# Kernel optimization log

Measured on AMD Instinct MI355X. Metric: run time of the kernel, lower is better.

Reference implementation:

```python
import jax, jax.numpy as jnp
import numpy as np

N, E = 20000, 4096
IN_DIM, DET_DIM, HID, OUT = 512, 256, 256, 2
HALF = HID // 2
EPS = 1e-6


def setup_inputs() -> dict:
    key = jax.random.key(0)
    ks = jax.random.split(key, 20)
    g = lambda k, shape, fan_in: jax.random.normal(k, shape, jnp.float32) / np.sqrt(fan_in)
    return {
        "x": jax.random.normal(ks[0], (N, IN_DIM), jnp.float32),
        "z": jax.random.normal(ks[1], (N, DET_DIM), jnp.float32),
        "incidence": jax.random.uniform(ks[2], (N, E), jnp.float32),
        "edge_weights": jax.random.uniform(ks[3], (E,), jnp.float32),
        "psi_w": g(ks[4], (IN_DIM, HALF), IN_DIM), "psi_b": jnp.zeros((HALF,), jnp.float32),
        "phi_w": g(ks[5], (DET_DIM, HALF), DET_DIM), "phi_b": jnp.zeros((HALF,), jnp.float32),
        "g1_w": g(ks[6], (2 * HALF, HID), 2 * HALF), "g1_b": jnp.zeros((HID,), jnp.float32),
        "g2_w": g(ks[7], (HID, HALF), HID), "g2_b": jnp.zeros((HALF,), jnp.float32),
        "th1": g(ks[8], (HALF, HID), HALF), "b1": jnp.zeros((HID,), jnp.float32),
        "th2": g(ks[9], (HID, HID), HID), "b2": jnp.zeros((HID,), jnp.float32),
        "out_w": g(ks[10], (HID, OUT), HID), "out_b": jnp.zeros((OUT,), jnp.float32),
    }


def hconv(X, H, w, theta, bias):
    # HGNN-style message passing: Dv^{-1/2} H W De^{-1} H^T Dv^{-1/2} (X theta) + b
    Xt = X @ theta                              # [N,F]
    De = H.sum(axis=0)                          # [E] edge degree
    Dv = H @ w                                  # [N] weighted node degree
    inv_sqrt_dv = jax.lax.rsqrt(jnp.maximum(Dv, EPS))[:, None]
    He = H.T @ (Xt * inv_sqrt_dv)               # [E,F] gather to hyperedges
    He = He * (w / jnp.maximum(De, EPS))[:, None]
    return (H @ He) * inv_sqrt_dv + bias        # scatter back to nodes


def reference(x, z, incidence, edge_weights,
              psi_w, psi_b, phi_w, phi_b,
              g1_w, g1_b, g2_w, g2_b,
              th1, b1, th2, b2, out_w, out_b):
    proj_x = x @ psi_w + psi_b                  # [N,HALF]
    proj_z = z @ phi_w + phi_b                  # [N,HALF]
    cat = jnp.concatenate([proj_x, proj_z], axis=1)
    gate = jax.nn.sigmoid(jax.nn.relu(cat @ g1_w + g1_b) @ g2_w + g2_b)
    fused = gate * proj_z + (1.0 - gate) * proj_x
    h = jax.nn.relu(hconv(fused, incidence, edge_weights, th1, b1))
    h = jax.nn.relu(hconv(h, incidence, edge_weights, th2, b2))
    logits = h @ out_w + out_b                  # [N,OUT]
    return logits, gate
```

## Files before the change

### kernel.cpp

```cpp
#include <hip/hip_runtime.h>
#include <hip/hip_bf16.h>


typedef __bf16 bf16_t;
typedef __attribute__((ext_vector_type(8))) __bf16 bf16x8;
typedef __attribute__((ext_vector_type(4))) __bf16 bf16x4;
typedef __attribute__((ext_vector_type(4))) float f32x4;

#define NN 20000
#define NE 4096
#define NNP 20480
#define AT_S 16
#define NEB 8
#define NNB 160

__device__ __forceinline__ f32x4 mfma16(bf16x8 a, bf16x8 b, f32x4 c) {
  return __builtin_amdgcn_mfma_f32_16x16x32_bf16(a, b, c, 0, 0, 0);
}

__global__ __launch_bounds__(256) void stats_cvt_kern(const float* __restrict__ H,
                                                      const float* __restrict__ w,
                                                      float* __restrict__ Dvp,
                                                      float* __restrict__ Dep,
                                                      bf16_t* __restrict__ Hbp) {
  __shared__ float dvl[128][17];
  __shared__ float deP[4][512];
  int t = threadIdx.x, l = t & 63, wv = t >> 6;
  long e0 = (long)blockIdx.x * 512;
  long n0 = (long)blockIdx.y * 128;
  long pA = ((e0 >> 6) + (l >> 4)) * (long)NNP;
  long pB = pA + 4 * (long)NNP;
  int inner = (l & 15) * 4;
  f32x4 wa = *(const f32x4*)(w + e0 + l * 4);
  f32x4 wb = *(const f32x4*)(w + e0 + 256 + l * 4);
  f32x4 dea; dea[0] = dea[1] = dea[2] = dea[3] = 0.f;
  f32x4 deb; deb[0] = deb[1] = deb[2] = deb[3] = 0.f;
  #pragma unroll 4
  for (int i = 0; i < 32; ++i) {
    long row = n0 + wv * 32 + i;
    float s;
    if (row < NN) {
      f32x4 ua = *(const f32x4*)(H + row * NE + e0 + l * 4);
      f32x4 ub = *(const f32x4*)(H + row * NE + e0 + 256 + l * 4);
      bf16x4 pa, pb;
      #pragma unroll
      for (int j = 0; j < 4; ++j) { pa[j] = (__bf16)ua[j]; pb[j] = (__bf16)ub[j]; }
      *(bf16x4*)(Hbp + (pA + row) * 64 + inner) = pa;
      *(bf16x4*)(Hbp + (pB + row) * 64 + inner) = pb;
      dea += ua; deb += ub;
      s = ua[0]*wa[0] + ua[1]*wa[1] + ua[2]*wa[2] + ua[3]*wa[3]
        + ub[0]*wb[0] + ub[1]*wb[1] + ub[2]*wb[2] + ub[3]*wb[3];
    } else {
      bf16x4 z;
      #pragma unroll
      for (int j = 0; j < 4; ++j) z[j] = (__bf16)0.f;
      *(bf16x4*)(Hbp + (pA + row) * 64 + inner) = z;
      *(bf16x4*)(Hbp + (pB + row) * 64 + inner) = z;
      s = 0.f;
    }
    s += __shfl_xor(s, 1);
    s += __shfl_xor(s, 2);
    if ((l & 3) == 0) dvl[wv * 32 + i][l >> 2] = s;
  }
  *(f32x4*)(&deP[wv][l * 4]) = dea;
  *(f32x4*)(&deP[wv][256 + l * 4]) = deb;
  __syncthreads();
  if (t < 128) {
    float s = 0.f;
    #pragma unroll
    for (int j = 0; j < 16; ++j) s += dvl[t][j];
    Dvp[(long)blockIdx.x * NNP + n0 + t] = s;
  }
  {
    float s0 = deP[0][t] + deP[1][t] + deP[2][t] + deP[3][t];
    float s1 = deP[0][256 + t] + deP[1][256 + t] + deP[2][256 + t] + deP[3][256 + t];
    Dep[(long)blockIdx.y * NE + e0 + t] = s0;
    Dep[(long)blockIdx.y * NE + e0 + 256 + t] = s1;
  }
}

__global__ __launch_bounds__(256) void finalize_kern(const float* __restrict__ Dvp,
                                                     const float* __restrict__ Dep,
                                                     const float* __restrict__ w,
                                                     float* __restrict__ isd,
                                                     float* __restrict__ es) {
  int t = blockIdx.x * 256 + threadIdx.x;
  if (t < NN) {
    float s = 0.f;
    #pragma unroll
    for (int b = 0; b < NEB; ++b) s += Dvp[(long)b * NNP + t];
    isd[t] = rsqrtf(fmaxf(s, 1e-6f));
  }
  if (t < NE) {
    float s = 0.f;
    #pragma unroll 8
    for (int b = 0; b < NNB; ++b) s += Dep[(long)b * NE + t];
    es[t] = w[t] / fmaxf(s, 1e-6f);
  }
}

__global__ void cvtw_kern(const float* __restrict__ psi, const float* __restrict__ phi,
                          const float* __restrict__ g1,  const float* __restrict__ g2,
                          const float* __restrict__ th1, const float* __restrict__ th2,
                          bf16_t* dpsi, bf16_t* dphi, bf16_t* dg1, bf16_t* dg2,
                          bf16_t* dth1, bf16_t* dth2) {
  int t = blockIdx.x * 256 + threadIdx.x;
  if (t < 65536) {
    int nc = t >> 9, k = t & 511; dpsi[t] = (__bf16)psi[k * 128 + nc];
  } else if (t < 98304) {
    int i = t - 65536; int nc = i >> 8, k = i & 255; dphi[i] = (__bf16)phi[k * 128 + nc];
  } else if (t < 163840) {
    int i = t - 98304; int nc = i >> 8, k = i & 255; dg1[i] = (__bf16)g1[k * 256 + nc];
  } else if (t < 196608) {
    int i = t - 163840; int nc = i >> 8, k = i & 255; dg2[i] = (__bf16)g2[k * 128 + nc];
  } else if (t < 229376) {
    int i = t - 196608; int nc = i >> 7, k = i & 127; dth1[i] = (__bf16)th1[k * 256 + nc];
  } else if (t < 294912) {
    int i = t - 229376; int nc = i >> 8, k = i & 255; dth2[i] = (__bf16)th2[k * 256 + nc];
  }
}

enum { EPI_CAT = 0, EPI_RELU = 1 };

template<bool AF32, int EPI>
__global__ __launch_bounds__(256) void gemm_node_kern(
    const void* __restrict__ Av, int lda, const bf16_t* __restrict__ Bt, int K,
    const float* __restrict__ bias, bf16_t* __restrict__ dst, int ldc) {
  int tid = threadIdx.x, l = tid & 63, wv = tid >> 6;
  int lr = l & 15, lq = l >> 4;
  int hm = wv >> 1;
  int mo = blockIdx.x * 32 + hm * 16;
  int no = blockIdx.y * 128 + (wv & 1) * 64;
  f32x4 acc[4] = {};
  for (int k0 = 0; k0 < K; k0 += 32) {
    int row = mo + lr;
    bf16x8 a;
    if (row < NN) {
      if constexpr (AF32) {
        const float* ap = (const float*)Av + (long)row * lda + k0 + lq * 8;
        f32x4 u0 = *(const f32x4*)ap, u1 = *(const f32x4*)(ap + 4);
        #pragma unroll
        for (int j = 0; j < 4; ++j) { a[j] = (__bf16)u0[j]; a[j + 4] = (__bf16)u1[j]; }
      } else {
        a = *(const bf16x8*)((const bf16_t*)Av + (long)row * lda + k0 + lq * 8);
      }
    } else {
      #pragma unroll
      for (int j = 0; j < 8; ++j) a[j] = (__bf16)0.f;
    }
    #pragma unroll
    for (int ni = 0; ni < 4; ++ni) {
      bf16x8 b = *(const bf16x8*)(Bt + (long)(no + ni * 16 + lr) * K + k0 + lq * 8);
      acc[ni] = mfma16(a, b, acc[ni]);
    }
  }
  #pragma unroll
  for (int ni = 0; ni < 4; ++ni) {
    int colf = no + ni * 16 + lr;
    int rb = mo + lq * 4;
    f32x4 v = acc[ni];
    float bs = bias[colf];
    for (int r = 0; r < 4; ++r) {
      int n = rb + r;
      if (n < NN) {
        float xx = v[r] + bs;
        if constexpr (EPI == EPI_RELU) xx = xx > 0.f ? xx : 0.f;
        dst[(long)n * ldc + colf] = (__bf16)xx;
      }
    }
  }
}

__global__ __launch_bounds__(256) void gate_y_kern(
    const bf16_t* __restrict__ hid1, const bf16_t* __restrict__ g2w,
    const float* __restrict__ g2b, const bf16_t* __restrict__ cat,
    const bf16_t* __restrict__ th1w, const float* __restrict__ isd,
    float* __restrict__ gate_out, bf16_t* __restrict__ Yf) {
  __shared__ bf16_t fl[32 * 132];
  int t = threadIdx.x, l = t & 63, wv = t >> 6;
  int lr = l & 15, lq = l >> 4;
  if (blockIdx.x >= 625) {
    bf16x8 z;
    #pragma unroll
    for (int j = 0; j < 8; ++j) z[j] = (__bf16)0.f;
    #pragma unroll
    for (int i = 0; i < 4; ++i)
      *(bf16x8*)(Yf + (((long)(wv + i * 4) * 640 + blockIdx.x) * 64 + l) * 8) = z;
    return;
  }
  long n0 = (long)blockIdx.x * 32;
  int hm = wv >> 1, nq = wv & 1;
  int mo = hm * 16, no = nq * 64;
  f32x4 acc[4] = {};
  for (int k0 = 0; k0 < 256; k0 += 32) {
    bf16x8 a = *(const bf16x8*)(hid1 + (n0 + mo + lr) * 256 + k0 + lq * 8);
    #pragma unroll
    for (int ni = 0; ni < 4; ++ni) {
      bf16x8 b = *(const bf16x8*)(g2w + (long)(no + ni * 16 + lr) * 256 + k0 + lq * 8);
      acc[ni] = mfma16(a, b, acc[ni]);
    }
  }
  #pragma unroll
  for (int ni = 0; ni < 4; ++ni) {
    int colf = no + ni * 16 + lr;
    float bs = g2b[colf];
    #pragma unroll
    for (int r = 0; r < 4; ++r) {
      long n = n0 + mo + lq * 4 + r;
      float g = 1.f / (1.f + __expf(-(acc[ni][r] + bs)));
      gate_out[n * 128 + colf] = g;
      float px = (float)cat[n * 256 + colf];
      float pz = (float)cat[n * 256 + 128 + colf];
      fl[(mo + lq * 4 + r) * 132 + colf] = (__bf16)(g * pz + (1.f - g) * px);
    }
  }
  __syncthreads();
  int hm2 = wv >> 1, f128 = (wv & 1) * 128;
  f32x4 acc2[8] = {};
  for (int k0 = 0; k0 < 128; k0 += 32) {
    bf16x8 a = *(const bf16x8*)(fl + (hm2 * 16 + lr) * 132 + k0 + lq * 8);
    #pragma unroll
    for (int ni = 0; ni < 8; ++ni) {
      bf16x8 b = *(const bf16x8*)(th1w + (long)(f128 + ni * 16 + lr) * 128 + k0 + lq * 8);
      acc2[ni] = mfma16(a, b, acc2[ni]);
    }
  }
  int lanep = (hm2 * 2 + (lq >> 1)) * 16 + lr;
  #pragma unroll
  for (int ni = 0; ni < 8; ++ni) {
    int fblk = (f128 >> 4) + ni;
    bf16x4 pk;
    #pragma unroll
    for (int r = 0; r < 4; ++r) {
      long n = n0 + hm2 * 16 + lq * 4 + r;
      pk[r] = (__bf16)(acc2[ni][r] * isd[n]);
    }
    *(bf16x4*)(Yf + (((long)fblk * 640 + blockIdx.x) * 64 + lanep) * 8 + (lq & 1) * 4) = pk;
  }
}

__global__ __launch_bounds__(512) void at_gemm_kern(const bf16_t* __restrict__ Hbp,
                                                    const bf16_t* __restrict__ Yf,
                                                    bf16_t* __restrict__ part) {
  __shared__ bf16_t T[128 * 72];
  int t = threadIdx.x, l = t & 63, wv = t >> 6;
  int lr = l & 15, lq = l >> 4;
  int eh = wv >> 2, fq = wv & 3;
  int e0 = blockIdx.x * 128;
  int s0 = blockIdx.y * 20, s1 = s0 + 20;
  int rp = t >> 4;
  int ck = t & 15;
  f32x4 acc[4][4] = {};
  const bf16_t* src = Hbp + (((long)(e0 >> 6) + (ck >> 3)) * NNP + (long)s0 * 64 + 2 * rp) * 64
                          + (ck & 7) * 8;
  bf16x8 ra = *(const bf16x8*)src;
  bf16x8 rb = *(const bf16x8*)(src + 64);
  for (int s = s0; s < s1; ++s) {
    __syncthreads();
    #pragma unroll
    for (int j = 0; j < 8; ++j) {
      int jj = (j + ck) & 7;
      int el = ck * 8 + jj;
      unsigned lo = (unsigned)__builtin_bit_cast(unsigned short, (__bf16)ra[jj]);
      unsigned hi = (unsigned)__builtin_bit_cast(unsigned short, (__bf16)rb[jj]);
      *(unsigned*)(T + el * 72 + rp * 2) = lo | (hi << 16);
    }
    __syncthreads();
    if (s + 1 < s1) {
      src += 64 * 64;
      ra = *(const bf16x8*)src;
      rb = *(const bf16x8*)(src + 64);
    }
    #pragma unroll
    for (int k32 = 0; k32 < 2; ++k32) {
      bf16x8 a[4], b[4];
      #pragma unroll
      for (int ni = 0; ni < 4; ++ni)
        a[ni] = *(const bf16x8*)(T + (eh * 64 + ni * 16 + lr) * 72 + k32 * 32 + lq * 8);
      const bf16_t* bp = Yf + ((long)(s * 2 + k32) * 64 + l) * 8;
      #pragma unroll
      for (int ni = 0; ni < 4; ++ni)
        b[ni] = *(const bf16x8*)(bp + (long)(fq * 4 + ni) * 640 * 512);
      #pragma unroll
      for (int ae = 0; ae < 4; ++ae)
        #pragma unroll
        for (int bf = 0; bf < 4; ++bf)
          acc[ae][bf] = mfma16(a[ae], b[bf], acc[ae][bf]);
    }
  }
  bf16_t* pp = part + (long)blockIdx.y * (256 * 4096);
  #pragma unroll
  for (int ae = 0; ae < 4; ++ae) {
    int eblk16 = (e0 >> 4) + eh * 4 + ae;
    #pragma unroll
    for (int bf = 0; bf < 4; ++bf) {
      int fblk = fq * 4 + bf;
      f32x4 v = acc[ae][bf];
      bf16x4 pk;
      for (int r = 0; r < 4; ++r) pk[r] = (__bf16)v[r];
      *(bf16x4*)(pp + (((long)eblk16 * 16 + fblk) * 64 + l) * 4) = pk;
    }
  }
}

__global__ __launch_bounds__(256) void reduce_he(const bf16_t* __restrict__ part,
                                                 const float* __restrict__ es,
                                                 bf16_t* __restrict__ Hef) {
  int u = blockIdx.x * 256 + threadIdx.x;
  int lane = u & 63, tile = u >> 6;
  int fblk = tile & 15, eblk16 = tile >> 4;
  int lr = lane & 15, lq = lane >> 4;
  int e_base = eblk16 * 16 + lq * 4;
  float a0 = 0.f, a1 = 0.f, a2 = 0.f, a3 = 0.f;
  #pragma unroll
  for (int s = 0; s < AT_S; ++s) {
    bf16x4 v = *(const bf16x4*)(part + (long)s * (256 * 4096) + (long)u * 4);
    a0 += (float)v[0]; a1 += (float)v[1]; a2 += (float)v[2]; a3 += (float)v[3];
  }
  f32x4 e4 = *(const f32x4*)(es + e_base);
  bf16x4 pk;
  pk[0] = (__bf16)(a0 * e4[0]); pk[1] = (__bf16)(a1 * e4[1]);
  pk[2] = (__bf16)(a2 * e4[2]); pk[3] = (__bf16)(a3 * e4[3]);
  int eblk32 = eblk16 >> 1;
  int lanep = ((eblk16 & 1) * 2 + (lq >> 1)) * 16 + lr;
  long slot = (((long)fblk * 128 + eblk32) * 64 + lanep) * 8 + (lq & 1) * 4;
  *(bf16x4*)(Hef + slot) = pk;
}

template<int CONV>
__global__ __launch_bounds__(512) void out_gemm_kern(const bf16_t* __restrict__ Hef,
                                                     const bf16_t* __restrict__ Hbp,
                                                     const float* __restrict__ isd,
                                                     const float* __restrict__ bias,
                                                     const bf16_t* __restrict__ th2w,
                                                     bf16_t* __restrict__ Yf,
                                                     const float* __restrict__ ow,
                                                     const float* __restrict__ ob,
                                                     float* __restrict__ out) {
  __shared__ bf16_t lbuf[2][5120];
  __shared__ float lgp[8][80][2];
  __shared__ bf16_t hl[80 * 260];
  int t = threadIdx.x, l = t & 63, wv = t >> 6;
  int lr = l & 15, lq = l >> 4;
  long r0 = (long)blockIdx.x * 80;
  f32x4 acc[5][2] = {};
  int f1 = wv, f2 = 8 + wv;
  bool has2 = wv < 2;
  const bf16_t* asrc1 = Hbp + (r0 + (f1 >> 1) * 16 + lr) * 64 + (f1 & 1) * 32 + lq * 8;
  const bf16_t* asrc2 = Hbp + (r0 + (f2 >> 1) * 16 + lr) * 64 + (f2 & 1) * 32 + lq * 8;
  const bf16_t* bbase = Hef + (long)l * 8;
  bf16x8 rg1 = *(const bf16x8*)asrc1;
  bf16x8 rg2;
  if (has2) rg2 = *(const bf16x8*)asrc2;
  int c = 0;
  for (int s = 0; s < 64; ++s) {
    *(bf16x8*)(&lbuf[c][f1 * 512 + l * 8]) = rg1;
    if (has2) *(bf16x8*)(&lbuf[c][f2 * 512 + l * 8]) = rg2;
    __syncthreads();
    if (s + 1 < 64) {
      rg1 = *(const bf16x8*)(asrc1 + (long)(s + 1) * NNP * 64);
      if (has2) rg2 = *(const bf16x8*)(asrc2 + (long)(s + 1) * NNP * 64);
    }
    #pragma unroll
    for (int k32 = 0; k32 < 2; ++k32) {
      bf16x8 a[5], b[2];
      #pragma unroll
      for (int mi = 0; mi < 5; ++mi)
        a[mi] = *(const bf16x8*)(&lbuf[c][(mi * 2 + k32) * 512 + l * 8]);
      int eblk = s * 2 + k32;
      #pragma unroll
      for (int ni = 0; ni < 2; ++ni)
        b[ni] = *(const bf16x8*)(bbase + ((long)(wv * 2 + ni) * 128 + eblk) * 512);
      #pragma unroll
      for (int mi = 0; mi < 5; ++mi) {
        acc[mi][0] = mfma16(a[mi], b[0], acc[mi][0]);
        acc[mi][1] = mfma16(a[mi], b[1], acc[mi][1]);
      }
    }
    c ^= 1;
  }
  #pragma unroll
  for (int mi = 0; mi < 5; ++mi) {
    long nb = r0 + mi * 16 + lq * 4;
    #pragma unroll
    for (int r = 0; r < 4; ++r) {
      long n = nb + r;
      float sd = (n < NN) ? isd[n] : 0.f;
      float a0 = 0.f, a1 = 0.f;
      #pragma unroll
      for (int ni = 0; ni < 2; ++ni) {
        int f = wv * 32 + ni * 16 + lr;
        float vv = acc[mi][ni][r] * sd + bias[f];
        vv = vv > 0.f ? vv : 0.f;
        if constexpr (CONV == 1) {
          hl[(mi * 16 + lq * 4 + r) * 260 + f] = (__bf16)vv;
        } else {
          a0 += vv * ow[f * 2];
          a1 += vv * ow[f * 2 + 1];
        }
      }
      if constexpr (CONV == 2) {
        #pragma unroll
        for (int m = 1; m < 16; m <<= 1) { a0 += __shfl_xor(a0, m); a1 += __shfl_xor(a1, m); }
        if (lr == 0) {
          int rowl = mi * 16 + lq * 4 + r;
          lgp[wv][rowl][0] = a0;
          lgp[wv][rowl][1] = a1;
        }
      }
    }
  }
  if constexpr (CONV == 1) {
    __syncthreads();
    f32x4 acc2[5][2] = {};
    for (int k0 = 0; k0 < 256; k0 += 32) {
      bf16x8 a_[5], b2[2];
      #pragma unroll
      for (int mi = 0; mi < 5; ++mi)
        a_[mi] = *(const bf16x8*)(hl + (mi * 16 + lr) * 260 + k0 + lq * 8);
      #pragma unroll
      for (int ni = 0; ni < 2; ++ni)
        b2[ni] = *(const bf16x8*)(th2w + (long)(wv * 32 + ni * 16 + lr) * 256 + k0 + lq * 8);
      #pragma unroll
      for (int mi = 0; mi < 5; ++mi) {
        acc2[mi][0] = mfma16(a_[mi], b2[0], acc2[mi][0]);
        acc2[mi][1] = mfma16(a_[mi], b2[1], acc2[mi][1]);
      }
    }
    #pragma unroll
    for (int mi = 0; mi < 5; ++mi) {
      long nbase = r0 + mi * 16;
      long nblk = nbase >> 5;
      int hm16 = (int)((nbase >> 4) & 1);
      int lanep = (hm16 * 2 + (lq >> 1)) * 16 + lr;
      #pragma unroll
      for (int ni = 0; ni < 2; ++ni) {
        int fblk = wv * 2 + ni;
        bf16x4 pk;
        #pragma unroll
        for (int r = 0; r < 4; ++r) {
          long n = nbase + lq * 4 + r;
          float sc = (n < NN) ? isd[n] : 0.f;
          pk[r] = (__bf16)(acc2[mi][ni][r] * sc);
        }
        *(bf16x4*)(Yf + (((long)fblk * 640 + nblk) * 64 + lanep) * 8 + (lq & 1) * 4) = pk;
      }
    }
  } else {
    __syncthreads();
    if (t < 80) {
      float s0 = 0.f, s1 = 0.f;
      #pragma unroll
      for (int wvi = 0; wvi < 8; ++wvi) { s0 += lgp[wvi][t][0]; s1 += lgp[wvi][t][1]; }
      long n = r0 + t;
      if (n < NN) {
        out[n * 2]     = s0 + ob[0];
        out[n * 2 + 1] = s1 + ob[1];
      }
    }
  }
}

extern "C" void kernel_launch(void* const* d_in, const int* in_sizes, int n_in,
                              void* d_out, int out_size, void* d_ws, size_t ws_size,
                              hipStream_t stream) {
  const float* x    = (const float*)d_in[0];
  const float* z    = (const float*)d_in[1];
  const float* H    = (const float*)d_in[2];
  const float* w    = (const float*)d_in[3];
  const float* psi_w = (const float*)d_in[4];
  const float* psi_b = (const float*)d_in[5];
  const float* phi_w = (const float*)d_in[6];
  const float* phi_b = (const float*)d_in[7];
  const float* g1_w  = (const float*)d_in[8];
  const float* g1_b  = (const float*)d_in[9];
  const float* g2_w  = (const float*)d_in[10];
  const float* g2_b  = (const float*)d_in[11];
  const float* th1   = (const float*)d_in[12];
  const float* b1    = (const float*)d_in[13];
  const float* th2   = (const float*)d_in[14];
  const float* b2    = (const float*)d_in[15];
  const float* out_w = (const float*)d_in[16];
  const float* out_b = (const float*)d_in[17];

  float* logits_out = (float*)d_out;
  float* gate_out   = logits_out + (size_t)NN * 2;

  char* p = (char*)d_ws;
  auto alloc = [&](size_t bytes) { char* r = p; p += (bytes + 255) & ~(size_t)255; return r; };
  float* Dvp  = (float*)alloc((size_t)NEB * NNP * 4);
  float* Dep  = (float*)alloc((size_t)NNB * NE * 4);
  float* isd  = (float*)alloc((size_t)NN * 4);
  float* es   = (float*)alloc((size_t)NE * 4);
  bf16_t* cat   = (bf16_t*)alloc((size_t)NN * 256 * 2);
  bf16_t* hid1  = (bf16_t*)alloc((size_t)NN * 256 * 2);
  bf16_t* Yf    = (bf16_t*)alloc((size_t)16 * 640 * 512 * 2);
  bf16_t* Hef   = (bf16_t*)alloc((size_t)16 * 128 * 512 * 2);
  bf16_t* pbuf  = (bf16_t*)alloc((size_t)AT_S * 256 * 4096 * 2);
  bf16_t* Hbp   = (bf16_t*)alloc((size_t)NNP * NE * 2);
  bf16_t* psi_wt = (bf16_t*)alloc(65536 * 2);
  bf16_t* phi_wt = (bf16_t*)alloc(32768 * 2);
  bf16_t* g1_wt  = (bf16_t*)alloc(65536 * 2);
  bf16_t* g2_wt  = (bf16_t*)alloc(32768 * 2);
  bf16_t* th1_wt = (bf16_t*)alloc(32768 * 2);
  bf16_t* th2_wt = (bf16_t*)alloc(65536 * 2);

  cvtw_kern<<<1152, 256, 0, stream>>>(psi_w, phi_w, g1_w, g2_w, th1, th2,
                                      psi_wt, phi_wt, g1_wt, g2_wt, th1_wt, th2_wt);
  stats_cvt_kern<<<dim3(NEB, NNB), 256, 0, stream>>>(H, w, Dvp, Dep, Hbp);
  finalize_kern<<<79, 256, 0, stream>>>(Dvp, Dep, w, isd, es);

  gemm_node_kern<true,  EPI_CAT ><<<dim3(625, 1), 256, 0, stream>>>(x, 512, psi_wt, 512, psi_b, cat,       256);
  gemm_node_kern<true,  EPI_CAT ><<<dim3(625, 1), 256, 0, stream>>>(z, 256, phi_wt, 256, phi_b, cat + 128, 256);
  gemm_node_kern<false, EPI_RELU><<<dim3(625, 2), 256, 0, stream>>>(cat, 256, g1_wt, 256, g1_b, hid1, 256);
  gate_y_kern<<<640, 256, 0, stream>>>(hid1, g2_wt, g2_b, cat, th1_wt, isd, gate_out, Yf);

  at_gemm_kern<<<dim3(32, AT_S), 512, 0, stream>>>(Hbp, Yf, pbuf);
  reduce_he<<<1024, 256, 0, stream>>>(pbuf, es, Hef);
  out_gemm_kern<1><<<256, 512, 0, stream>>>(Hef, Hbp, isd, b1, th2_wt, Yf,
                                            nullptr, nullptr, nullptr);

  at_gemm_kern<<<dim3(32, AT_S), 512, 0, stream>>>(Hbp, Yf, pbuf);
  reduce_he<<<1024, 256, 0, stream>>>(pbuf, es, Hef);
  out_gemm_kern<2><<<256, 512, 0, stream>>>(Hef, Hbp, isd, b2, nullptr, nullptr,
                                            out_w, out_b, logits_out);

  (void)in_sizes; (void)n_in; (void)out_size; (void)ws_size;
}
```

Measured before the change: 537.1 us.

## Merge independent prologue kernels and double-buffer LDS in hyperedge gather GEMM

The incidence-stats/bf16 conversion kernel is merged with the x/z projection GEMMs into one launch. The degree finalize step is merged with the gate hidden GEMM into a second launch, dispatched by block index. This cuts the kernel count and lets the independent work overlap. Separately, the at_gemm kernel now double-buffers its LDS transpose tile, so each step needs one barrier instead of two and the next tile's write overlaps the current MFMAs. The cost is twice the LDS in at_gemm, which could lower occupancy.

```diff
diff --git a/kernel.cpp b/kernel.cpp
--- a/kernel.cpp
+++ b/kernel.cpp
@@ -18,16 +18,13 @@
   return __builtin_amdgcn_mfma_f32_16x16x32_bf16(a, b, c, 0, 0, 0);
 }
 
-__global__ __launch_bounds__(256) void stats_cvt_kern(const float* __restrict__ H,
-                                                      const float* __restrict__ w,
-                                                      float* __restrict__ Dvp,
-                                                      float* __restrict__ Dep,
-                                                      bf16_t* __restrict__ Hbp) {
-  __shared__ float dvl[128][17];
-  __shared__ float deP[4][512];
+__device__ __forceinline__ void stats_body(int vbx, int vby,
+    const float* __restrict__ H, const float* __restrict__ w,
+    float* __restrict__ Dvp, float* __restrict__ Dep, bf16_t* __restrict__ Hbp,
+    float (*dvl)[17], float (*deP)[512]) {
   int t = threadIdx.x, l = t & 63, wv = t >> 6;
-  long e0 = (long)blockIdx.x * 512;
-  long n0 = (long)blockIdx.y * 128;
+  long e0 = (long)vbx * 512;
+  long n0 = (long)vby * 128;
   long pA = ((e0 >> 6) + (l >> 4)) * (long)NNP;
   long pB = pA + 4 * (long)NNP;
   int inner = (l & 15) * 4;
@@ -69,33 +66,131 @@
     float s = 0.f;
     #pragma unroll
     for (int j = 0; j < 16; ++j) s += dvl[t][j];
-    Dvp[(long)blockIdx.x * NNP + n0 + t] = s;
+    Dvp[(long)vbx * NNP + n0 + t] = s;
   }
   {
     float s0 = deP[0][t] + deP[1][t] + deP[2][t] + deP[3][t];
     float s1 = deP[0][256 + t] + deP[1][256 + t] + deP[2][256 + t] + deP[3][256 + t];
-    Dep[(long)blockIdx.y * NE + e0 + t] = s0;
-    Dep[(long)blockIdx.y * NE + e0 + 256 + t] = s1;
-  }
-}
-
-__global__ __launch_bounds__(256) void finalize_kern(const float* __restrict__ Dvp,
-                                                     const float* __restrict__ Dep,
-                                                     const float* __restrict__ w,
-                                                     float* __restrict__ isd,
-                                                     float* __restrict__ es) {
-  int t = blockIdx.x * 256 + threadIdx.x;
-  if (t < NN) {
-    float s = 0.f;
-    #pragma unroll
-    for (int b = 0; b < NEB; ++b) s += Dvp[(long)b * NNP + t];
-    isd[t] = rsqrtf(fmaxf(s, 1e-6f));
-  }
-  if (t < NE) {
-    float s = 0.f;
-    #pragma unroll 8
-    for (int b = 0; b < NNB; ++b) s += Dep[(long)b * NE + t];
-    es[t] = w[t] / fmaxf(s, 1e-6f);
+    Dep[(long)vby * NE + e0 + t] = s0;
+    Dep[(long)vby * NE + e0 + 256 + t] = s1;
+  }
+}
+
+__device__ __forceinline__ void cat_gemm_body(const float* __restrict__ Av, int lda,
+    const bf16_t* __restrict__ Bt, int K, const float* __restrict__ bias,
+    bf16_t* __restrict__ dst, int vbx) {
+  int tid = threadIdx.x, l = tid & 63, wv = tid >> 6;
+  int lr = l & 15, lq = l >> 4;
+  int mo = vbx * 32 + (wv >> 1) * 16;
+  int no = (wv & 1) * 64;
+  f32x4 acc[4] = {};
+  for (int k0 = 0; k0 < K; k0 += 32) {
+    int row = mo + lr;
+    bf16x8 a;
+    if (row < NN) {
+      const float* ap = Av + (long)row * lda + k0 + lq * 8;
+      f32x4 u0 = *(const f32x4*)ap, u1 = *(const f32x4*)(ap + 4);
+      #pragma unroll
+      for (int j = 0; j < 4; ++j) { a[j] = (__bf16)u0[j]; a[j + 4] = (__bf16)u1[j]; }
+    } else {
+      #pragma unroll
+      for (int j = 0; j < 8; ++j) a[j] = (__bf16)0.f;
+    }
+    #pragma unroll
+    for (int ni = 0; ni < 4; ++ni) {
+      bf16x8 b = *(const bf16x8*)(Bt + (long)(no + ni * 16 + lr) * K + k0 + lq * 8);
+      acc[ni] = mfma16(a, b, acc[ni]);
+    }
+  }
+  #pragma unroll
+  for (int ni = 0; ni < 4; ++ni) {
+    int colf = no + ni * 16 + lr;
+    int rb = mo + lq * 4;
+    float bs = bias[colf];
+    #pragma unroll
+    for (int r = 0; r < 4; ++r) {
+      int n = rb + r;
+      if (n < NN) dst[(long)n * 256 + colf] = (__bf16)(acc[ni][r] + bs);
+    }
+  }
+}
+
+__global__ __launch_bounds__(256) void fusedA_kern(const float* __restrict__ H,
+    const float* __restrict__ w, float* __restrict__ Dvp, float* __restrict__ Dep,
+    bf16_t* __restrict__ Hbp,
+    const float* __restrict__ x, const bf16_t* __restrict__ psi_wt,
+    const float* __restrict__ psi_b,
+    const float* __restrict__ z, const bf16_t* __restrict__ phi_wt,
+    const float* __restrict__ phi_b, bf16_t* __restrict__ cat) {
+  __shared__ float dvl[128][17];
+  __shared__ float deP[4][512];
+  int bid = blockIdx.x;
+  if (bid < 1280) {
+    stats_body(bid & 7, bid >> 3, H, w, Dvp, Dep, Hbp, dvl, deP);
+  } else if (bid < 1905) {
+    cat_gemm_body(x, 512, psi_wt, 512, psi_b, cat, bid - 1280);
+  } else {
+    cat_gemm_body(z, 256, phi_wt, 256, phi_b, cat + 128, bid - 1905);
+  }
+}
+
+__global__ __launch_bounds__(256) void fusedB_kern(const float* __restrict__ Dvp,
+    const float* __restrict__ Dep, const float* __restrict__ w,
+    float* __restrict__ isd, float* __restrict__ es,
+    const bf16_t* __restrict__ cat, const bf16_t* __restrict__ g1w,
+    const float* __restrict__ g1b, bf16_t* __restrict__ hid1) {
+  int bid = blockIdx.x;
+  if (bid < 79) {
+    int t = bid * 256 + threadIdx.x;
+    if (t < NN) {
+      float s = 0.f;
+      #pragma unroll
+      for (int b = 0; b < NEB; ++b) s += Dvp[(long)b * NNP + t];
+      isd[t] = rsqrtf(fmaxf(s, 1e-6f));
+    }
+    if (t < NE) {
+      float s = 0.f;
+      #pragma unroll 8
+      for (int b = 0; b < NNB; ++b) s += Dep[(long)b * NE + t];
+      es[t] = w[t] / fmaxf(s, 1e-6f);
+    }
+    return;
+  }
+  int i = bid - 79;
+  int vbx = i % 625, vby = i / 625;
+  int tid = threadIdx.x, l = tid & 63, wv = tid >> 6;
+  int lr = l & 15, lq = l >> 4;
+  int mo = vbx * 32 + (wv >> 1) * 16;
+  int no = vby * 128 + (wv & 1) * 64;
+  f32x4 acc[4] = {};
+  for (int k0 = 0; k0 < 256; k0 += 32) {
+    int row = mo + lr;
+    bf16x8 a;
+    if (row < NN) {
+      a = *(const bf16x8*)(cat + (long)row * 256 + k0 + lq * 8);
+    } else {
+      #pragma unroll
+      for (int j = 0; j < 8; ++j) a[j] = (__bf16)0.f;
+    }
+    #pragma unroll
+    for (int ni = 0; ni < 4; ++ni) {
+      bf16x8 b = *(const bf16x8*)(g1w + (long)(no + ni * 16 + lr) * 256 + k0 + lq * 8);
+      acc[ni] = mfma16(a, b, acc[ni]);
+    }
+  }
+  #pragma unroll
+  for (int ni = 0; ni < 4; ++ni) {
+    int colf = no + ni * 16 + lr;
+    int rb = mo + lq * 4;
+    float bs = g1b[colf];
+    #pragma unroll
+    for (int r = 0; r < 4; ++r) {
+      int n = rb + r;
+      if (n < NN) {
+        float xx = acc[ni][r] + bs;
+        hid1[(long)n * 256 + colf] = (__bf16)(xx > 0.f ? xx : 0.f);
+      }
+    }
   }
 }
 
@@ -120,57 +215,6 @@
   }
 }
 
-enum { EPI_CAT = 0, EPI_RELU = 1 };
-
-template<bool AF32, int EPI>
-__global__ __launch_bounds__(256) void gemm_node_kern(
-    const void* __restrict__ Av, int lda, const bf16_t* __restrict__ Bt, int K,
-    const float* __restrict__ bias, bf16_t* __restrict__ dst, int ldc) {
-  int tid = threadIdx.x, l = tid & 63, wv = tid >> 6;
-  int lr = l & 15, lq = l >> 4;
-  int hm = wv >> 1;
-  int mo = blockIdx.x * 32 + hm * 16;
-  int no = blockIdx.y * 128 + (wv & 1) * 64;
-  f32x4 acc[4] = {};
-  for (int k0 = 0; k0 < K; k0 += 32) {
-    int row = mo + lr;
-    bf16x8 a;
-    if (row < NN) {
-      if constexpr (AF32) {
-        const float* ap = (const float*)Av + (long)row * lda + k0 + lq * 8;
-        f32x4 u0 = *(const f32x4*)ap, u1 = *(const f32x4*)(ap + 4);
-        #pragma unroll
-        for (int j = 0; j < 4; ++j) { a[j] = (__bf16)u0[j]; a[j + 4] = (__bf16)u1[j]; }
-      } else {
-        a = *(const bf16x8*)((const bf16_t*)Av + (long)row * lda + k0 + lq * 8);
-      }
-    } else {
-      #pragma unroll
-      for (int j = 0; j < 8; ++j) a[j] = (__bf16)0.f;
-    }
-    #pragma unroll
-    for (int ni = 0; ni < 4; ++ni) {
-      bf16x8 b = *(const bf16x8*)(Bt + (long)(no + ni * 16 + lr) * K + k0 + lq * 8);
-      acc[ni] = mfma16(a, b, acc[ni]);
-    }
-  }
-  #pragma unroll
-  for (int ni = 0; ni < 4; ++ni) {
-    int colf = no + ni * 16 + lr;
-    int rb = mo + lq * 4;
-    f32x4 v = acc[ni];
-    float bs = bias[colf];
-    for (int r = 0; r < 4; ++r) {
-      int n = rb + r;
-      if (n < NN) {
-        float xx = v[r] + bs;
-        if constexpr (EPI == EPI_RELU) xx = xx > 0.f ? xx : 0.f;
-        dst[(long)n * ldc + colf] = (__bf16)xx;
-      }
-    }
-  }
-}
-
 __global__ __launch_bounds__(256) void gate_y_kern(
     const bf16_t* __restrict__ hid1, const bf16_t* __restrict__ g2w,
     const float* __restrict__ g2b, const bf16_t* __restrict__ cat,
@@ -242,12 +286,12 @@
 __global__ __launch_bounds__(512) void at_gemm_kern(const bf16_t* __restrict__ Hbp,
                                                     const bf16_t* __restrict__ Yf,
                                                     bf16_t* __restrict__ part) {
-  __shared__ bf16_t T[128 * 72];
+  __shared__ bf16_t T[2][128 * 72];
   int t = threadIdx.x, l = t & 63, wv = t >> 6;
   int lr = l & 15, lq = l >> 4;
   int eh = wv >> 2, fq = wv & 3;
   int e0 = blockIdx.x * 128;
-  int s0 = blockIdx.y * 20, s1 = s0 + 20;
+  int s0 = blockIdx.y * 20;
   int rp = t >> 4;
   int ck = t & 15;
   f32x4 acc[4][4] = {};
@@ -255,28 +299,45 @@
                           + (ck & 7) * 8;
   bf16x8 ra = *(const bf16x8*)src;
   bf16x8 rb = *(const bf16x8*)(src + 64);
-  for (int s = s0; s < s1; ++s) {
-    __syncthreads();
+  {
     #pragma unroll
     for (int j = 0; j < 8; ++j) {
       int jj = (j + ck) & 7;
       int el = ck * 8 + jj;
       unsigned lo = (unsigned)__builtin_bit_cast(unsigned short, (__bf16)ra[jj]);
       unsigned hi = (unsigned)__builtin_bit_cast(unsigned short, (__bf16)rb[jj]);
-      *(unsigned*)(T + el * 72 + rp * 2) = lo | (hi << 16);
-    }
+      *(unsigned*)(&T[0][el * 72 + rp * 2]) = lo | (hi << 16);
+    }
+    src += 64 * 64;
+    ra = *(const bf16x8*)src;
+    rb = *(const bf16x8*)(src + 64);
+  }
+  for (int i = 0; i < 20; ++i) {
     __syncthreads();
-    if (s + 1 < s1) {
+    if (i + 1 < 20) {
+      int nb = (i + 1) & 1;
+      #pragma unroll
+      for (int j = 0; j < 8; ++j) {
+        int jj = (j + ck) & 7;
+        int el = ck * 8 + jj;
+        unsigned lo = (unsigned)__builtin_bit_cast(unsigned short, (__bf16)ra[jj]);
+        unsigned hi = (unsigned)__builtin_bit_cast(unsigned short, (__bf16)rb[jj]);
+        *(unsigned*)(&T[nb][el * 72 + rp * 2]) = lo | (hi << 16);
+      }
+    }
+    if (i + 2 < 20) {
       src += 64 * 64;
       ra = *(const bf16x8*)src;
       rb = *(const bf16x8*)(src + 64);
     }
+    int cb = i & 1;
+    int s = s0 + i;
     #pragma unroll
     for (int k32 = 0; k32 < 2; ++k32) {
       bf16x8 a[4], b[4];
       #pragma unroll
       for (int ni = 0; ni < 4; ++ni)
-        a[ni] = *(const bf16x8*)(T + (eh * 64 + ni * 16 + lr) * 72 + k32 * 32 + lq * 8);
+        a[ni] = *(const bf16x8*)(&T[cb][(eh * 64 + ni * 16 + lr) * 72 + k32 * 32 + lq * 8]);
       const bf16_t* bp = Yf + ((long)(s * 2 + k32) * 64 + l) * 8;
       #pragma unroll
       for (int ni = 0; ni < 4; ++ni)
@@ -507,12 +568,10 @@
 
   cvtw_kern<<<1152, 256, 0, stream>>>(psi_w, phi_w, g1_w, g2_w, th1, th2,
                                       psi_wt, phi_wt, g1_wt, g2_wt, th1_wt, th2_wt);
-  stats_cvt_kern<<<dim3(NEB, NNB), 256, 0, stream>>>(H, w, Dvp, Dep, Hbp);
-  finalize_kern<<<79, 256, 0, stream>>>(Dvp, Dep, w, isd, es);
-
-  gemm_node_kern<true,  EPI_CAT ><<<dim3(625, 1), 256, 0, stream>>>(x, 512, psi_wt, 512, psi_b, cat,       256);
-  gemm_node_kern<true,  EPI_CAT ><<<dim3(625, 1), 256, 0, stream>>>(z, 256, phi_wt, 256, phi_b, cat + 128, 256);
-  gemm_node_kern<false, EPI_RELU><<<dim3(625, 2), 256, 0, stream>>>(cat, 256, g1_wt, 256, g1_b, hid1, 256);
+  fusedA_kern<<<2530, 256, 0, stream>>>(H, w, Dvp, Dep, Hbp,
+                                        x, psi_wt, psi_b, z, phi_wt, phi_b, cat);
+  fusedB_kern<<<1329, 256, 0, stream>>>(Dvp, Dep, w, isd, es,
+                                        cat, g1_wt, g1_b, hid1);
   gate_y_kern<<<640, 256, 0, stream>>>(hid1, g2_wt, g2_b, cat, th1_wt, isd, gate_out, Yf);
 
   at_gemm_kern<<<dim3(32, AT_S), 512, 0, stream>>>(Hbp, Yf, pbuf);
```

Result: faster. 507.1 us, median of 2 (-5.6%).
